# Kernel tuning notes

Measured on AMD Instinct MI355X. Metric: run time of the kernel, lower is better.

Reference implementation:

```python
import jax, jax.numpy as jnp
import numpy as np

B, NF, T, N = 64, 64, 8192, 1024  # batch, n_formants, frames, tokens


def setup_inputs() -> dict:
    key = jax.random.key(0)
    kx, kd = jax.random.split(key)
    x = jax.random.normal(kx, (B, NF, T), dtype=jnp.float32)
    # durations: nonneg ints whose cumsum stays within [0, T]
    ends = jnp.sort(jax.random.randint(kd, (B, N), 0, T + 1), axis=1)
    durations = jnp.diff(ends, axis=1, prepend=jnp.zeros((B, 1), dtype=ends.dtype)).astype(jnp.int64)
    return {"x": x, "durations": durations}


def reference(x, durations):
    # x: [B, NF, T], durations: [B, N]
    dce = jnp.cumsum(durations, axis=1).astype(jnp.int32)          # [B, N] segment ends
    dcs = jnp.pad(dce[:, :-1], ((0, 0), (1, 0)))                   # [B, N] segment starts
    # padded inclusive cumsums along time -> exclusive prefix sums of length T+1
    x_cums = jnp.pad(jnp.cumsum(x, axis=2), ((0, 0), (0, 0), (1, 0)))                    # [B, NF, T+1]
    x_nz_cums = jnp.pad(jnp.cumsum((x != 0.0).astype(x.dtype), axis=2), ((0, 0), (0, 0), (1, 0)))
    b, nf, n = x.shape[0], x.shape[1], durations.shape[1]
    dce_b = jnp.broadcast_to(dce[:, None, :], (b, nf, n))
    dcs_b = jnp.broadcast_to(dcs[:, None, :], (b, nf, n))
    x_sums = jnp.take_along_axis(x_cums, dce_b, axis=2) - jnp.take_along_axis(x_cums, dcs_b, axis=2)
    x_nelems = jnp.take_along_axis(x_nz_cums, dce_b, axis=2) - jnp.take_along_axis(x_nz_cums, dcs_b, axis=2)
    return jnp.where(x_nelems == 0.0, x_nelems, x_sums / x_nelems)  # [B, NF, N]
```

## Files before the change

### kernel.cpp

```cpp
#include <hip/hip_runtime.h>

#define BB 64
#define NF 64
#define TT 8192
#define NN 1024
#define G  (TT / 4)
#define PAD(c) ((c) + ((c) >> 3))
#define CSZ (PAD(G) + 1)

__global__ __launch_bounds__(256, 5) void fused_kernel(const float* __restrict__ x,
                                                       const int* __restrict__ dur,
                                                       float* __restrict__ out) {
    const int row  = blockIdx.x;
    const int b    = row >> 6;
    const int t    = threadIdx.x;
    const int lane = t & 63;
    const int w    = t >> 6;

    __shared__ int   bs[NN + 1];
    __shared__ float csum[CSZ];
    __shared__ int   ccnt[CSZ];
    __shared__ float P[NN + 1];
    __shared__ float Kc[NN + 1];
    __shared__ float wsf[4];
    __shared__ int   wsi[4];

    const int4 d4 = ((const int4*)(dur + b * NN))[t];
    const int s0 = d4.x, s1 = s0 + d4.y, s2 = s1 + d4.z, s3 = s2 + d4.w;
    int wsum = s3;
#pragma unroll
    for (int d = 1; d < 64; d <<= 1) {
        int u = __shfl_up(wsum, d, 64);
        if (lane >= d) wsum += u;
    }
    if (lane == 63) wsi[w] = wsum;
    __syncthreads();
    int boff = 0;
#pragma unroll
    for (int i = 0; i < 4; ++i) if (i < w) boff += wsi[i];
    const int ebase = boff + wsum - s3;
    bs[4 * t + 1] = ebase + s0;
    bs[4 * t + 2] = ebase + s1;
    bs[4 * t + 3] = ebase + s2;
    bs[4 * t + 4] = ebase + s3;
    if (t == 0) bs[0] = 0;
    __syncthreads();

    const float4* __restrict__ xv = (const float4*)(x + (size_t)row * TT);
#pragma unroll
    for (int k = 0; k < G / 256; ++k) {
        const int c = t + (k << 8);
        const float4 v = xv[c];
        csum[PAD(c)] = v.x + v.y + v.z + v.w;
        ccnt[PAD(c)] = (v.x != 0.f) + (v.y != 0.f) + (v.z != 0.f) + (v.w != 0.f);
    }

    for (int i = t; i <= NN; i += 256) {
        const int p = bs[i];
        const int g = p >> 2, r = p & 3;
        float part = 0.f, pc = 0.f;
        if (r) {
            const float4 v = xv[g];
            part = v.x; pc = (v.x != 0.f);
            if (r > 1) { part += v.y; pc += (v.y != 0.f); }
            if (r > 2) { part += v.z; pc += (v.z != 0.f); }
        }
        P[i] = part; Kc[i] = pc;
    }
    __syncthreads();

    float sv[8]; int cv[8];
    float fs = 0.f; int cs = 0;
#pragma unroll
    for (int j = 0; j < 8; ++j) {
        const int c = (t << 3) + j;
        fs += csum[PAD(c)];
        cs += ccnt[PAD(c)];
        sv[j] = fs; cv[j] = cs;
    }
    float ws = fs; int wc = cs;
#pragma unroll
    for (int d = 1; d < 64; d <<= 1) {
        float uf = __shfl_up(ws, d, 64);
        int   ui = __shfl_up(wc, d, 64);
        if (lane >= d) { ws += uf; wc += ui; }
    }
    if (lane == 63) { wsf[w] = ws; wsi[w] = wc; }
    __syncthreads();
    float woff = 0.f; int coff = 0;
#pragma unroll
    for (int i = 0; i < 4; ++i) if (i < w) { woff += wsf[i]; coff += wsi[i]; }
    const float fbase = woff + (ws - fs);
    const int   cbase = coff + (wc - cs);
#pragma unroll
    for (int j = 0; j < 8; ++j) {
        const int c = (t << 3) + j;
        csum[PAD(c)] = fbase + (j ? sv[j - 1] : 0.f);
        ccnt[PAD(c)] = cbase + (j ? cv[j - 1] : 0);
    }
    if (t == 255) { csum[PAD(G)] = woff + ws; ccnt[PAD(G)] = coff + wc; }
    __syncthreads();

    for (int i = t; i <= NN; i += 256) {
        const int g = bs[i] >> 2;
        P[i]  += csum[PAD(g)];
        Kc[i] += (float)ccnt[PAD(g)];
    }
    __syncthreads();

    float* orow = out + (size_t)row * NN;
#pragma unroll
    for (int k = 0; k < NN / 256; ++k) {
        const int n = t + (k << 8);
        const float s = P[n + 1] - P[n];
        const float c = Kc[n + 1] - Kc[n];
        orow[n] = (c != 0.f) ? (s / c) : 0.f;
    }
}

extern "C" void kernel_launch(void* const* d_in, const int* in_sizes, int n_in,
                              void* d_out, int out_size, void* d_ws, size_t ws_size,
                              hipStream_t stream) {
    const float* x   = (const float*)d_in[0];
    const int*   dur = (const int*)d_in[1];
    float*       out = (float*)d_out;
    fused_kernel<<<BB * NF, 256, 0, stream>>>(x, dur, out);
}
```

Measured before the change: 206.8 us.

## Split into streaming group-reduce kernel and per-row scan finalize kernel

Moves the per-8-element sum and nonzero-count reduction into a separate fully parallel streaming kernel that writes partial results to workspace. A second kernel scans these partials per row and gathers the boundary remainders from x. This is meant to raise memory-level parallelism and shrink the per-row block's LDS and serial work, at the cost of extra global traffic for the intermediate buffer and a second launch. Counts also change from int to float accumulation.

```diff
diff --git a/kernel.cpp b/kernel.cpp
--- a/kernel.cpp
+++ b/kernel.cpp
@@ -4,30 +4,44 @@
 #define NF 64
 #define TT 8192
 #define NN 1024
-#define G  (TT / 4)
+#define GR 8
+#define NG (TT / GR)
+#define ROWS (BB * NF)
 #define PAD(c) ((c) + ((c) >> 3))
-#define CSZ (PAD(G) + 1)
 
-__global__ __launch_bounds__(256, 5) void fused_kernel(const float* __restrict__ x,
+__global__ __launch_bounds__(256) void reduce_kernel(const float* __restrict__ x,
+                                                     float2* __restrict__ gsc) {
+    const size_t tid = (size_t)blockIdx.x * 256 + threadIdx.x;
+    const float4* xp = (const float4*)(x + tid * GR);
+    const float4 a = xp[0], b = xp[1];
+    const float s = ((a.x + a.y) + (a.z + a.w)) + ((b.x + b.y) + (b.z + b.w));
+    const float c = ((a.x != 0.f) + (a.y != 0.f) + (a.z != 0.f) + (a.w != 0.f))
+                  + ((b.x != 0.f) + (b.y != 0.f) + (b.z != 0.f) + (b.w != 0.f));
+    gsc[tid] = make_float2(s, c);
+}
+
+__global__ __launch_bounds__(256) void finalize_kernel(const float* __restrict__ x,
                                                        const int* __restrict__ dur,
+                                                       const float2* __restrict__ gsc,
                                                        float* __restrict__ out) {
     const int row  = blockIdx.x;
-    const int b    = row >> 6;
+    const int bat  = row >> 6;
     const int t    = threadIdx.x;
     const int lane = t & 63;
     const int w    = t >> 6;
 
     __shared__ int   bs[NN + 1];
-    __shared__ float csum[CSZ];
-    __shared__ int   ccnt[CSZ];
+    __shared__ float S[PAD(NG) + 1];
+    __shared__ float C[PAD(NG) + 1];
     __shared__ float P[NN + 1];
     __shared__ float Kc[NN + 1];
     __shared__ float wsf[4];
+    __shared__ float wcf[4];
     __shared__ int   wsi[4];
 
-    const int4 d4 = ((const int4*)(dur + b * NN))[t];
-    const int s0 = d4.x, s1 = s0 + d4.y, s2 = s1 + d4.z, s3 = s2 + d4.w;
-    int wsum = s3;
+    const int4 d4 = ((const int4*)(dur + bat * NN))[t];
+    const int i0 = d4.x, i1 = i0 + d4.y, i2 = i1 + d4.z, i3 = i2 + d4.w;
+    int wsum = i3;
 #pragma unroll
     for (int d = 1; d < 64; d <<= 1) {
         int u = __shfl_up(wsum, d, 64);
@@ -38,73 +52,65 @@
     int boff = 0;
 #pragma unroll
     for (int i = 0; i < 4; ++i) if (i < w) boff += wsi[i];
-    const int ebase = boff + wsum - s3;
-    bs[4 * t + 1] = ebase + s0;
-    bs[4 * t + 2] = ebase + s1;
-    bs[4 * t + 3] = ebase + s2;
-    bs[4 * t + 4] = ebase + s3;
+    const int eb = boff + wsum - i3;
+    bs[4 * t + 1] = eb + i0;
+    bs[4 * t + 2] = eb + i1;
+    bs[4 * t + 3] = eb + i2;
+    bs[4 * t + 4] = eb + i3;
     if (t == 0) bs[0] = 0;
+
+    const float4* grow = (const float4*)(gsc + (size_t)row * NG);
+    const float4 ga = grow[2 * t];
+    const float4 gb = grow[2 * t + 1];
+    float sv[4], cv[4];
+    sv[0] = ga.x;         cv[0] = ga.y;
+    sv[1] = sv[0] + ga.z; cv[1] = cv[0] + ga.w;
+    sv[2] = sv[1] + gb.x; cv[2] = cv[1] + gb.y;
+    sv[3] = sv[2] + gb.z; cv[3] = cv[2] + gb.w;
+    float ws = sv[3], wc = cv[3];
+#pragma unroll
+    for (int d = 1; d < 64; d <<= 1) {
+        float uf = __shfl_up(ws, d, 64);
+        float uc = __shfl_up(wc, d, 64);
+        if (lane >= d) { ws += uf; wc += uc; }
+    }
+    if (lane == 63) { wsf[w] = ws; wcf[w] = wc; }
+    __syncthreads();
+    float woff = 0.f, coff = 0.f;
+#pragma unroll
+    for (int i = 0; i < 4; ++i) if (i < w) { woff += wsf[i]; coff += wcf[i]; }
+    const float fbase = woff + (ws - sv[3]);
+    const float cbase = coff + (wc - cv[3]);
+#pragma unroll
+    for (int j = 0; j < 4; ++j) {
+        const int c = 4 * t + j;
+        S[PAD(c)] = fbase + (j ? sv[j - 1] : 0.f);
+        C[PAD(c)] = cbase + (j ? cv[j - 1] : 0.f);
+    }
+    if (t == 255) { S[PAD(NG)] = woff + ws; C[PAD(NG)] = coff + wc; }
     __syncthreads();
 
-    const float4* __restrict__ xv = (const float4*)(x + (size_t)row * TT);
-#pragma unroll
-    for (int k = 0; k < G / 256; ++k) {
-        const int c = t + (k << 8);
-        const float4 v = xv[c];
-        csum[PAD(c)] = v.x + v.y + v.z + v.w;
-        ccnt[PAD(c)] = (v.x != 0.f) + (v.y != 0.f) + (v.z != 0.f) + (v.w != 0.f);
-    }
-
+    const float* xrow = x + (size_t)row * TT;
     for (int i = t; i <= NN; i += 256) {
         const int p = bs[i];
-        const int g = p >> 2, r = p & 3;
+        const int g = p >> 3, r = p & 7;
         float part = 0.f, pc = 0.f;
         if (r) {
-            const float4 v = xv[g];
+            const float* xb = xrow + (p & ~7);
+            const float4 v = *(const float4*)xb;
             part = v.x; pc = (v.x != 0.f);
             if (r > 1) { part += v.y; pc += (v.y != 0.f); }
             if (r > 2) { part += v.z; pc += (v.z != 0.f); }
+            if (r > 3) { part += v.w; pc += (v.w != 0.f); }
+            if (r > 4) {
+                const float4 u = *(const float4*)(xb + 4);
+                part += u.x; pc += (u.x != 0.f);
+                if (r > 5) { part += u.y; pc += (u.y != 0.f); }
+                if (r > 6) { part += u.z; pc += (u.z != 0.f); }
+            }
         }
-        P[i] = part; Kc[i] = pc;
-    }
-    __syncthreads();
-
-    float sv[8]; int cv[8];
-    float fs = 0.f; int cs = 0;
-#pragma unroll
-    for (int j = 0; j < 8; ++j) {
-        const int c = (t << 3) + j;
-        fs += csum[PAD(c)];
-        cs += ccnt[PAD(c)];
-        sv[j] = fs; cv[j] = cs;
-    }
-    float ws = fs; int wc = cs;
-#pragma unroll
-    for (int d = 1; d < 64; d <<= 1) {
-        float uf = __shfl_up(ws, d, 64);
-        int   ui = __shfl_up(wc, d, 64);
-        if (lane >= d) { ws += uf; wc += ui; }
-    }
-    if (lane == 63) { wsf[w] = ws; wsi[w] = wc; }
-    __syncthreads();
-    float woff = 0.f; int coff = 0;
-#pragma unroll
-    for (int i = 0; i < 4; ++i) if (i < w) { woff += wsf[i]; coff += wsi[i]; }
-    const float fbase = woff + (ws - fs);
-    const int   cbase = coff + (wc - cs);
-#pragma unroll
-    for (int j = 0; j < 8; ++j) {
-        const int c = (t << 3) + j;
-        csum[PAD(c)] = fbase + (j ? sv[j - 1] : 0.f);
-        ccnt[PAD(c)] = cbase + (j ? cv[j - 1] : 0);
-    }
-    if (t == 255) { csum[PAD(G)] = woff + ws; ccnt[PAD(G)] = coff + wc; }
-    __syncthreads();
-
-    for (int i = t; i <= NN; i += 256) {
-        const int g = bs[i] >> 2;
-        P[i]  += csum[PAD(g)];
-        Kc[i] += (float)ccnt[PAD(g)];
+        P[i]  = S[PAD(g)] + part;
+        Kc[i] = C[PAD(g)] + pc;
     }
     __syncthreads();
 
@@ -124,5 +130,8 @@
     const float* x   = (const float*)d_in[0];
     const int*   dur = (const int*)d_in[1];
     float*       out = (float*)d_out;
-    fused_kernel<<<BB * NF, 256, 0, stream>>>(x, dur, out);
+    float2*      gsc = (float2*)d_ws;
+
+    reduce_kernel<<<ROWS * NG / 256, 256, 0, stream>>>(x, gsc);
+    finalize_kernel<<<ROWS, 256, 0, stream>>>(x, dur, gsc, out);
 }
```

Result: slower. 227.4 us (+10.0%).

## Stage row in shared memory, keep boundaries in registers, vectorize output stores

Applied to the files above, without the earlier changes.

The kernel now loads the whole x row into registers up front and copies it to a new shared buffer, so the partial-group lookups at segment boundaries read shared memory instead of issuing scattered global loads. Segment boundaries stay in registers, one thread per four consecutive tokens, which removes the boundary shared array, one sync pass, and the P/Kc arrays. Output is written as one float4 per thread, and sum and count are packed as float2 so each prefix-scan access is a single LDS. In exchange the block uses about 32KB more LDS and the launch-bounds occupancy hint is dropped, which may reduce blocks per CU.

```diff
diff --git a/kernel.cpp b/kernel.cpp
--- a/kernel.cpp
+++ b/kernel.cpp
@@ -4,30 +4,31 @@
 #define NF 64
 #define TT 8192
 #define NN 1024
-#define G  (TT / 4)
+#define NC (TT / 4)
 #define PAD(c) ((c) + ((c) >> 3))
-#define CSZ (PAD(G) + 1)
 
-__global__ __launch_bounds__(256, 5) void fused_kernel(const float* __restrict__ x,
-                                                       const int* __restrict__ dur,
-                                                       float* __restrict__ out) {
+__global__ __launch_bounds__(256) void fused_kernel(const float* __restrict__ x,
+                                                    const int* __restrict__ dur,
+                                                    float* __restrict__ out) {
     const int row  = blockIdx.x;
-    const int b    = row >> 6;
+    const int bat  = row >> 6;
     const int t    = threadIdx.x;
     const int lane = t & 63;
     const int w    = t >> 6;
 
-    __shared__ int   bs[NN + 1];
-    __shared__ float csum[CSZ];
-    __shared__ int   ccnt[CSZ];
-    __shared__ float P[NN + 1];
-    __shared__ float Kc[NN + 1];
-    __shared__ float wsf[4];
-    __shared__ int   wsi[4];
+    __shared__ float  raw[TT];
+    __shared__ float2 SC[PAD(NC) + 1];
+    __shared__ int    wsi[4];
+    __shared__ float  wsf[4], wcf[4];
 
-    const int4 d4 = ((const int4*)(dur + b * NN))[t];
-    const int s0 = d4.x, s1 = s0 + d4.y, s2 = s1 + d4.z, s3 = s2 + d4.w;
-    int wsum = s3;
+    const float4* __restrict__ xv = (const float4*)(x + (size_t)row * TT);
+    float4 stage[8];
+#pragma unroll
+    for (int k = 0; k < 8; ++k) stage[k] = xv[t + (k << 8)];
+    const int4 d4 = ((const int4*)(dur + bat * NN))[t];
+
+    const int i0 = d4.x, i1 = i0 + d4.y, i2 = i1 + d4.z, i3 = i2 + d4.w;
+    int wsum = i3;
 #pragma unroll
     for (int d = 1; d < 64; d <<= 1) {
         int u = __shfl_up(wsum, d, 64);
@@ -38,84 +39,76 @@
     int boff = 0;
 #pragma unroll
     for (int i = 0; i < 4; ++i) if (i < w) boff += wsi[i];
-    const int ebase = boff + wsum - s3;
-    bs[4 * t + 1] = ebase + s0;
-    bs[4 * t + 2] = ebase + s1;
-    bs[4 * t + 3] = ebase + s2;
-    bs[4 * t + 4] = ebase + s3;
-    if (t == 0) bs[0] = 0;
-    __syncthreads();
+    const int eb = boff + wsum - i3;
+    const int bnd[5] = { eb, eb + i0, eb + i1, eb + i2, eb + i3 };
 
-    const float4* __restrict__ xv = (const float4*)(x + (size_t)row * TT);
 #pragma unroll
-    for (int k = 0; k < G / 256; ++k) {
+    for (int k = 0; k < 8; ++k) {
         const int c = t + (k << 8);
-        const float4 v = xv[c];
-        csum[PAD(c)] = v.x + v.y + v.z + v.w;
-        ccnt[PAD(c)] = (v.x != 0.f) + (v.y != 0.f) + (v.z != 0.f) + (v.w != 0.f);
-    }
-
-    for (int i = t; i <= NN; i += 256) {
-        const int p = bs[i];
-        const int g = p >> 2, r = p & 3;
-        float part = 0.f, pc = 0.f;
-        if (r) {
-            const float4 v = xv[g];
-            part = v.x; pc = (v.x != 0.f);
-            if (r > 1) { part += v.y; pc += (v.y != 0.f); }
-            if (r > 2) { part += v.z; pc += (v.z != 0.f); }
-        }
-        P[i] = part; Kc[i] = pc;
+        ((float4*)raw)[c] = stage[k];
+        const float4 v = stage[k];
+        SC[PAD(c)] = make_float2(v.x + v.y + v.z + v.w,
+                                 (v.x != 0.f) + (v.y != 0.f) + (v.z != 0.f) + (v.w != 0.f));
     }
     __syncthreads();
 
-    float sv[8]; int cv[8];
-    float fs = 0.f; int cs = 0;
+    float sv[8], cv[8];
+    float fs = 0.f, cs = 0.f;
 #pragma unroll
     for (int j = 0; j < 8; ++j) {
-        const int c = (t << 3) + j;
-        fs += csum[PAD(c)];
-        cs += ccnt[PAD(c)];
+        const float2 p = SC[PAD((t << 3) + j)];
+        fs += p.x; cs += p.y;
         sv[j] = fs; cv[j] = cs;
     }
-    float ws = fs; int wc = cs;
+    float ws = fs, wc = cs;
 #pragma unroll
     for (int d = 1; d < 64; d <<= 1) {
         float uf = __shfl_up(ws, d, 64);
-        int   ui = __shfl_up(wc, d, 64);
-        if (lane >= d) { ws += uf; wc += ui; }
+        float uc = __shfl_up(wc, d, 64);
+        if (lane >= d) { ws += uf; wc += uc; }
     }
-    if (lane == 63) { wsf[w] = ws; wsi[w] = wc; }
+    if (lane == 63) { wsf[w] = ws; wcf[w] = wc; }
     __syncthreads();
-    float woff = 0.f; int coff = 0;
+    float woff = 0.f, coff = 0.f;
 #pragma unroll
-    for (int i = 0; i < 4; ++i) if (i < w) { woff += wsf[i]; coff += wsi[i]; }
-    const float fbase = woff + (ws - fs);
-    const int   cbase = coff + (wc - cs);
+    for (int i = 0; i < 4; ++i) if (i < w) { woff += wsf[i]; coff += wcf[i]; }
+    const float fb = woff + (ws - fs);
+    const float cb = coff + (wc - cs);
 #pragma unroll
     for (int j = 0; j < 8; ++j) {
-        const int c = (t << 3) + j;
-        csum[PAD(c)] = fbase + (j ? sv[j - 1] : 0.f);
-        ccnt[PAD(c)] = cbase + (j ? cv[j - 1] : 0);
+        SC[PAD((t << 3) + j)] = make_float2(fb + (j ? sv[j - 1] : 0.f),
+                                            cb + (j ? cv[j - 1] : 0.f));
     }
-    if (t == 255) { csum[PAD(G)] = woff + ws; ccnt[PAD(G)] = coff + wc; }
+    if (t == 255) SC[PAD(NC)] = make_float2(woff + ws, coff + wc);
     __syncthreads();
 
-    for (int i = t; i <= NN; i += 256) {
-        const int g = bs[i] >> 2;
-        P[i]  += csum[PAD(g)];
-        Kc[i] += (float)ccnt[PAD(g)];
+    float ps[5], pk[5];
+#pragma unroll
+    for (int j = 0; j < 5; ++j) {
+        const int p = bnd[j];
+        const int g = p >> 2, r = p & 3;
+        const float2 pre = SC[PAD(g)];
+        float s = pre.x, c = pre.y;
+        if (r) {
+            const float4 v = ((const float4*)raw)[g];
+            s += v.x; c += (v.x != 0.f);
+            if (r > 1) { s += v.y; c += (v.y != 0.f); }
+            if (r > 2) { s += v.z; c += (v.z != 0.f); }
+        }
+        ps[j] = s; pk[j] = c;
     }
-    __syncthreads();
-
-    float* orow = out + (size_t)row * NN;
-#pragma unroll
-    for (int k = 0; k < NN / 256; ++k) {
-        const int n = t + (k << 8);
-        const float s = P[n + 1] - P[n];
-        const float c = Kc[n + 1] - Kc[n];
-        orow[n] = (c != 0.f) ? (s / c) : 0.f;
+    float4 o;
+    {
+        const float s0 = ps[1] - ps[0], c0 = pk[1] - pk[0];
+        const float s1 = ps[2] - ps[1], c1 = pk[2] - pk[1];
+        const float s2 = ps[3] - ps[2], c2 = pk[3] - pk[2];
+        const float s3 = ps[4] - ps[3], c3 = pk[4] - pk[3];
+        o.x = (c0 != 0.f) ? s0 / c0 : 0.f;
+        o.y = (c1 != 0.f) ? s1 / c1 : 0.f;
+        o.z = (c2 != 0.f) ? s2 / c2 : 0.f;
+        o.w = (c3 != 0.f) ? s3 / c3 : 0.f;
     }
+    ((float4*)(out + (size_t)row * NN))[t] = o;
 }
 
 extern "C" void kernel_launch(void* const* d_in, const int* in_sizes, int n_in,
```

Measured after the change: 193.2 us. 6.6% less time.
